# Kernel optimization log

Hardware: AMD Instinct MI355X
Metric: run time of the kernel (lower is better)

The kernel has to match this reference:

```python
import jax, jax.numpy as jnp
import numpy as np

N_NODES = 50000


def _gcn_conv(x, src, dst, W, b, n_nodes):
    # x: [N, Fin] -> h: [N, Fout]; GCN: D^-1/2 (A+I) D^-1/2 (x W) + b
    h = x @ W
    deg = jax.ops.segment_sum(jnp.ones_like(dst, dtype=h.dtype), dst,
                              num_segments=n_nodes)
    dinv = jax.lax.rsqrt(jnp.maximum(deg, 1.0))
    norm = dinv[src] * dinv[dst]                      # [E]
    msg = h[src] * norm[:, None]                      # [E, Fout] gather
    agg = jax.ops.segment_sum(msg, dst, num_segments=n_nodes)  # scatter-add
    return agg + b


def setup_inputs() -> dict:
    key = jax.random.key(0)
    k0, k1, k2, k3 = jax.random.split(key, 4)
    N, E, F_IN, H, C = N_NODES, 800000, 128, 128, 16
    x = jax.random.normal(k0, (N, F_IN), dtype=jnp.float32)
    edge_index = jax.random.randint(k1, (2, E), 0, N, dtype=jnp.int64)
    W1 = jax.random.normal(k2, (F_IN, H), dtype=jnp.float32) / np.sqrt(F_IN)
    b1 = jnp.zeros((H,), dtype=jnp.float32)
    W2 = jax.random.normal(k3, (H, C), dtype=jnp.float32) / np.sqrt(H)
    b2 = jnp.zeros((C,), dtype=jnp.float32)
    return {"x": x, "edge_index": edge_index, "W1": W1, "b1": b1,
            "W2": W2, "b2": b2}


def reference(x, edge_index, W1, b1, W2, b2):
    n = x.shape[0]
    # add self-loops (shared by both conv layers)
    loops = jnp.arange(n, dtype=edge_index.dtype)
    src = jnp.concatenate([edge_index[0], loops])
    dst = jnp.concatenate([edge_index[1], loops])
    h = _gcn_conv(x, src, dst, W1, b1, n)
    h = jax.nn.relu(h)
    # dropout p=0.5 is identity in eval mode
    h = _gcn_conv(h, src, dst, W2, b2, n)
    return jax.nn.log_softmax(h, axis=1)
```

## Files before the change

### kernel.cpp

```cpp
#include <hip/hip_runtime.h>
#include <math.h>


#define NBUCKET_SHIFT 8
#define BIN_CHUNK 4096

typedef __bf16 bf16x8 __attribute__((ext_vector_type(8)));
typedef float  f32x4  __attribute__((ext_vector_type(4)));
typedef float  f32x2  __attribute__((ext_vector_type(2)));

__device__ __forceinline__ unsigned short pack_bf16(float f) {
    unsigned u = __float_as_uint(f);
    return (unsigned short)((u + 0x7fffu + ((u >> 16) & 1u)) >> 16);
}

__device__ __forceinline__ void acc_fp8x16(f32x2* a, uint4 v) {
    a[0] += __builtin_amdgcn_cvt_pk_f32_fp8(v.x, false);
    a[1] += __builtin_amdgcn_cvt_pk_f32_fp8(v.x, true);
    a[2] += __builtin_amdgcn_cvt_pk_f32_fp8(v.y, false);
    a[3] += __builtin_amdgcn_cvt_pk_f32_fp8(v.y, true);
    a[4] += __builtin_amdgcn_cvt_pk_f32_fp8(v.z, false);
    a[5] += __builtin_amdgcn_cvt_pk_f32_fp8(v.z, true);
    a[6] += __builtin_amdgcn_cvt_pk_f32_fp8(v.w, false);
    a[7] += __builtin_amdgcn_cvt_pk_f32_fp8(v.w, true);
}

__global__ __launch_bounds__(256)
void count_wt_kernel(const int* __restrict__ dst, int* __restrict__ bktcnt,
                     int E, int nbuckets, int nbins,
                     const float* __restrict__ W, unsigned short* __restrict__ wtp) {
    const int blk = blockIdx.x;
    const int tid = threadIdx.x;
    if (blk >= nbins) {
        int idx = (blk - nbins) * 256 + tid;
        int j    = idx & 7;
        int lane = (idx >> 3) & 63;
        int ks   = (idx >> 9) & 3;
        int t    = idx >> 11;
        int n = t * 16 + (lane & 15);
        int k = ks * 32 + ((lane >> 4) << 3) + j;
        wtp[idx] = pack_bf16(W[k * 128 + n]);
        return;
    }
    __shared__ int cnt[256];
    cnt[tid] = 0;
    __syncthreads();
    const int e0 = blk * BIN_CHUNK;
    const int n = min(BIN_CHUNK, E - e0);
    for (int i = tid; i < n; i += 256)
        atomicAdd(&cnt[dst[e0 + i] >> NBUCKET_SHIFT], 1);
    __syncthreads();
    if (tid < nbuckets && cnt[tid] > 0) atomicAdd(&bktcnt[tid], cnt[tid]);
}

__global__ __launch_bounds__(256)
void bin_kernel(const int* __restrict__ src, const int* __restrict__ dst,
                const int* __restrict__ bktcnt, int* __restrict__ bcur,
                unsigned* __restrict__ pairs, int E, int nbuckets) {
    __shared__ unsigned spair[BIN_CHUNK];
    __shared__ int lcnt[256];
    __shared__ int lbase[256];
    __shared__ int sbase[256];
    const int tid = threadIdx.x;
    const int e0 = blockIdx.x * BIN_CHUNK;
    const int cnt = min(BIN_CHUNK, E - e0);

    int v = (tid < nbuckets) ? bktcnt[tid] : 0;
    sbase[tid] = v;
    lcnt[tid] = 0;
    __syncthreads();
#pragma unroll
    for (int off = 1; off < 256; off <<= 1) {
        int u = (tid >= off) ? sbase[tid - off] : 0;
        __syncthreads();
        sbase[tid] += u;
        __syncthreads();
    }
    int excl = sbase[tid] - v;
    __syncthreads();
    sbase[tid] = excl;
    __syncthreads();

    for (int i = tid; i < cnt; i += 256) {
        unsigned s = (unsigned)src[e0 + i], d = (unsigned)dst[e0 + i];
        spair[i] = (d >> NBUCKET_SHIFT) << 24 | (d & 255u) << 16 | s;
        atomicAdd(&lcnt[d >> NBUCKET_SHIFT], 1);
    }
    __syncthreads();

    if (tid < nbuckets) {
        int c = lcnt[tid];
        lbase[tid] = (c > 0) ? atomicAdd(&bcur[tid], c) : 0;
        lcnt[tid] = 0;
    }
    __syncthreads();

    for (int i = tid; i < cnt; i += 256) {
        unsigned p = spair[i];
        int b = (int)(p >> 24);
        int off = atomicAdd(&lcnt[b], 1);
        pairs[sbase[b] + lbase[b] + off] = p;
    }
}

__global__ __launch_bounds__(256)
void bucket_build_kernel(const int* __restrict__ bktcnt, const unsigned* __restrict__ pairs,
                         int* __restrict__ rowptr, float* __restrict__ dinv,
                         int* __restrict__ colsrc, int N, int E, int nbuckets) {
    __shared__ int cnt[256];
    __shared__ int sm[256];
    const int tid = threadIdx.x;
    const int blk = blockIdx.x;
    const int nb0 = blk << NBUCKET_SHIFT;

    int bv = (tid < nbuckets) ? bktcnt[tid] : 0;
    sm[tid] = bv;
    cnt[tid] = 0;
    __syncthreads();
#pragma unroll
    for (int off = 1; off < 256; off <<= 1) {
        int u = (tid >= off) ? sm[tid - off] : 0;
        __syncthreads();
        sm[tid] += u;
        __syncthreads();
    }
    __syncthreads();
    const int hi0 = sm[blk];
    const int lo = hi0 - bktcnt[blk];
    const int hi = hi0;
    __syncthreads();

    for (int i = lo + tid; i < hi; i += 256)
        atomicAdd(&cnt[(int)(pairs[i] >> 16) & 255], 1);
    __syncthreads();

    int v = cnt[tid];
    sm[tid] = v;
    __syncthreads();
#pragma unroll
    for (int off = 1; off < 256; off <<= 1) {
        int u = (tid >= off) ? sm[tid - off] : 0;
        __syncthreads();
        sm[tid] += u;
        __syncthreads();
    }
    int excl = sm[tid] - v;
    int node = nb0 + tid;
    if (node < N) {
        rowptr[node] = lo + excl;
        dinv[node] = rsqrtf((float)v + 1.0f);
    }
    __syncthreads();
    cnt[tid] = lo + excl;
    __syncthreads();
    for (int i = lo + tid; i < hi; i += 256) {
        unsigned p = pairs[i];
        int pos = atomicAdd(&cnt[(int)(p >> 16) & 255], 1);
        colsrc[pos] = (int)(p & 0xffffu);
    }
    if (blk == 0 && tid == 0) rowptr[N] = E;
}

__global__ __launch_bounds__(256)
void gemm1_mfma_kernel(const float* __restrict__ x, const unsigned short* __restrict__ wtp,
                       const float* __restrict__ dinv, unsigned* __restrict__ h1b, int N) {
    __shared__ float lds[4][16 * 132];
    const int tid = threadIdx.x, wave = tid >> 6, lane = tid & 63;
    const int q = lane >> 4, m = lane & 15;
    const int row0 = blockIdx.x * 64 + wave * 16;
    const int row = row0 + m;
    const int rowc = (row < N) ? row : (N - 1);

    f32x4 acc[8];
#pragma unroll
    for (int t = 0; t < 8; t++) acc[t] = (f32x4)0.0f;

#pragma unroll
    for (int ks = 0; ks < 4; ks++) {
        const float4* xp = (const float4*)(x + (size_t)rowc * 128 + ks * 32 + q * 8);
        float4 f0 = xp[0], f1 = xp[1];
        float fv[8] = {f0.x, f0.y, f0.z, f0.w, f1.x, f1.y, f1.z, f1.w};
        bf16x8 ah, al;
#pragma unroll
        for (int j = 0; j < 8; j++) {
            __bf16 h = (__bf16)fv[j];
            ah[j] = h;
            al[j] = (__bf16)(fv[j] - (float)h);
        }
#pragma unroll
        for (int t = 0; t < 8; t++) {
            bf16x8 b = *(const bf16x8*)(wtp + (size_t)(t * 4 + ks) * 512 + lane * 8);
            acc[t] = __builtin_amdgcn_mfma_f32_16x16x32_bf16(ah, b, acc[t], 0, 0, 0);
            acc[t] = __builtin_amdgcn_mfma_f32_16x16x32_bf16(al, b, acc[t], 0, 0, 0);
        }
    }

#pragma unroll
    for (int t = 0; t < 8; t++)
#pragma unroll
        for (int r = 0; r < 4; r++)
            lds[wave][(q * 4 + r) * 132 + t * 16 + m] = acc[t][r];
    __syncthreads();

    const int r2 = lane >> 2, j = lane & 3;
    const int orow = row0 + r2;
    if (orow < N) {
        float dv = dinv[orow];
        const float* lrow = &lds[wave][r2 * 132];
#pragma unroll
        for (int s = 0; s < 4; s++) {
            float4 a = *(const float4*)(lrow + s * 32 + j * 8);
            float4 b = *(const float4*)(lrow + s * 32 + j * 8 + 4);
            unsigned lo = __builtin_amdgcn_cvt_pk_fp8_f32(a.x * dv, a.y * dv, 0, false);
            lo = __builtin_amdgcn_cvt_pk_fp8_f32(a.z * dv, a.w * dv, lo, true);
            unsigned hi = __builtin_amdgcn_cvt_pk_fp8_f32(b.x * dv, b.y * dv, 0, false);
            hi = __builtin_amdgcn_cvt_pk_fp8_f32(b.z * dv, b.w * dv, hi, true);
            ((uint2*)h1b)[(size_t)orow * 16 + s * 4 + j] = make_uint2(lo, hi);
        }
    }
}

__global__ __launch_bounds__(256)
void l1_fused_kernel(const int* __restrict__ rowptr, const int* __restrict__ colsrc,
                     const float* __restrict__ dinv, const unsigned* __restrict__ h1b,
                     const float* __restrict__ b1, const float* __restrict__ W2,
                     float* __restrict__ h2s, int N) {
    __shared__ float rows[4][2][132];
    __shared__ float w2s[128 * 16];
    const int tid = threadIdx.x;
    const int wave = tid >> 6, lane = tid & 63;
    const int c = lane & 7;
    const int g = (lane >> 3) & 3;
    const int n = lane >> 5;
    const int d = blockIdx.x * 8 + wave * 2 + n;

    for (int i = tid; i < 512; i += 256)
        ((float4*)w2s)[i] = ((const float4*)W2)[i];

    const uint4* hq = (const uint4*)h1b;

    if (d < N) {
        f32x2 a[8];
#pragma unroll
        for (int j = 0; j < 8; j++) a[j] = (f32x2)0.0f;

        if (g == 0)
            acc_fp8x16(a, hq[(size_t)d * 8 + c]);

        int i = rowptr[d], end = rowptr[d + 1];
        for (; i + 16 <= end; i += 16) {
            int s0 = colsrc[i + g],     s1 = colsrc[i + 4 + g];
            int s2 = colsrc[i + 8 + g], s3 = colsrc[i + 12 + g];
            uint4 v0 = hq[(size_t)s0 * 8 + c];
            uint4 v1 = hq[(size_t)s1 * 8 + c];
            uint4 v2 = hq[(size_t)s2 * 8 + c];
            uint4 v3 = hq[(size_t)s3 * 8 + c];
            acc_fp8x16(a, v0); acc_fp8x16(a, v1);
            acc_fp8x16(a, v2); acc_fp8x16(a, v3);
        }
        for (; i + 4 <= end; i += 4) {
            int sx = colsrc[i + g];
            acc_fp8x16(a, hq[(size_t)sx * 8 + c]);
        }
        if (i < end && g < end - i)
            acc_fp8x16(a, hq[(size_t)colsrc[i + g] * 8 + c]);

#pragma unroll
        for (int j = 0; j < 8; j++) {
            a[j].x += __shfl_xor(a[j].x, 8, 64);
            a[j].y += __shfl_xor(a[j].y, 8, 64);
            a[j].x += __shfl_xor(a[j].x, 16, 64);
            a[j].y += __shfl_xor(a[j].y, 16, 64);
        }

        if (g == 0) {
            float dv = dinv[d];
            float* rbase = &rows[wave][n][c * 16];
#pragma unroll
            for (int t = 0; t < 4; t++) {
                float4 bb = ((const float4*)b1)[c * 4 + t];
                float4 o;
                o.x = fmaxf(a[2 * t].x * dv + bb.x, 0.0f);
                o.y = fmaxf(a[2 * t].y * dv + bb.y, 0.0f);
                o.z = fmaxf(a[2 * t + 1].x * dv + bb.z, 0.0f);
                o.w = fmaxf(a[2 * t + 1].y * dv + bb.w, 0.0f);
                *(float4*)(rbase + 4 * t) = o;
            }
        }
    }
    __syncthreads();

    const int n2 = lane >> 5, kh = (lane >> 4) & 1, col = lane & 15;
    const int d2 = blockIdx.x * 8 + wave * 2 + n2;
    if (d2 < N) {
        const float* r = &rows[wave][n2][kh * 64];
        const float* w = &w2s[kh * 64 * 16];
        float p = 0.0f;
#pragma unroll
        for (int k = 0; k < 64; k++)
            p = fmaf(r[k], w[k * 16 + col], p);
        p += __shfl_xor(p, 16, 64);
        if (kh == 0) h2s[(size_t)d2 * 16 + col] = p * dinv[d2];
    }
}

__global__ __launch_bounds__(256)
void l2_kernel(const int* __restrict__ rowptr, const int* __restrict__ colsrc,
               const float* __restrict__ dinv, const float* __restrict__ h2s,
               const float* __restrict__ b2, float* __restrict__ out, int N) {
    const int tid = threadIdx.x;
    const int wave = tid >> 6, lane = tid & 63;
    const int g = lane >> 2;
    const int c = lane & 3;
    const int d = blockIdx.x * 4 + wave;
    if (d >= N) return;
    const float4* h2q = (const float4*)h2s;

    float4 acc = make_float4(0.f, 0.f, 0.f, 0.f);
    if (g == 0) acc = h2q[d * 4 + c];
    int i = rowptr[d], end = rowptr[d + 1];
    for (; i + 16 <= end; i += 16) {
        int s = colsrc[i + g];
        float4 v = h2q[s * 4 + c];
        acc.x += v.x; acc.y += v.y; acc.z += v.z; acc.w += v.w;
    }
    if (i < end && g < end - i) {
        int s = colsrc[i + g];
        float4 v = h2q[s * 4 + c];
        acc.x += v.x; acc.y += v.y; acc.z += v.z; acc.w += v.w;
    }
#pragma unroll
    for (int off = 4; off <= 32; off <<= 1) {
        acc.x += __shfl_xor(acc.x, off, 64);
        acc.y += __shfl_xor(acc.y, off, 64);
        acc.z += __shfl_xor(acc.z, off, 64);
        acc.w += __shfl_xor(acc.w, off, 64);
    }
    float dv = dinv[d];
    float4 b = ((const float4*)b2)[c];
    float4 val = make_float4(acc.x * dv + b.x, acc.y * dv + b.y,
                             acc.z * dv + b.z, acc.w * dv + b.w);
    float m = fmaxf(fmaxf(val.x, val.y), fmaxf(val.z, val.w));
    m = fmaxf(m, __shfl_xor(m, 1, 64));
    m = fmaxf(m, __shfl_xor(m, 2, 64));
    float e = expf(val.x - m) + expf(val.y - m) + expf(val.z - m) + expf(val.w - m);
    e += __shfl_xor(e, 1, 64);
    e += __shfl_xor(e, 2, 64);
    float lse = m + logf(e);
    if (g == 0)
        ((float4*)out)[d * 4 + c] =
            make_float4(val.x - lse, val.y - lse, val.z - lse, val.w - lse);
}

extern "C" void kernel_launch(void* const* d_in, const int* in_sizes, int n_in,
                              void* d_out, int out_size, void* d_ws, size_t ws_size,
                              hipStream_t stream) {
    const float* x  = (const float*)d_in[0];
    const int*  ei  = (const int*)d_in[1];
    const float* W1 = (const float*)d_in[2];
    const float* b1 = (const float*)d_in[3];
    const float* W2 = (const float*)d_in[4];
    const float* b2 = (const float*)d_in[5];
    float* out = (float*)d_out;

    const int N = in_sizes[0] / 128;
    const int E = in_sizes[1] / 2;
    const int* src = ei;
    const int* dst = ei + E;
    const int nbuckets = (N + 255) >> NBUCKET_SHIFT;
    const int nbins = (E + BIN_CHUNK - 1) / BIN_CHUNK;

    float*          wsf     = (float*)d_ws;
    float*          dinv    = wsf;
    int*            rowptr  = (int*)(wsf + N);
    int*            bktcnt  = rowptr + N + 4;
    int*            bcur    = bktcnt + 256;
    unsigned short* wtp     = (unsigned short*)(bcur + 256);
    int*            colsrc  = bcur + 256 + 8192;
    unsigned*       pairs   = (unsigned*)(colsrc + E);
    unsigned*       h1b     = pairs + E;
    float*          h2s     = (float*)(h1b + (size_t)N * 32);

    hipMemsetAsync(bktcnt, 0, 512 * sizeof(int), stream);
    count_wt_kernel<<<nbins + 64, 256, 0, stream>>>(dst, bktcnt, E, nbuckets,
                                                    nbins, W1, wtp);
    bin_kernel<<<nbins, 256, 0, stream>>>(src, dst, bktcnt, bcur, pairs, E, nbuckets);
    bucket_build_kernel<<<nbuckets, 256, 0, stream>>>(bktcnt, pairs, rowptr,
                                                      dinv, colsrc, N, E, nbuckets);

    gemm1_mfma_kernel<<<(N + 63) / 64, 256, 0, stream>>>(x, wtp, dinv, h1b, N);

    l1_fused_kernel<<<(N + 7) / 8, 256, 0, stream>>>(rowptr, colsrc, dinv, h1b,
                                                     b1, W2, h2s, N);

    l2_kernel<<<(N + 3) / 4, 256, 0, stream>>>(rowptr, colsrc, dinv, h2s, b2, out, N);
}
```

Baseline: 188.8 us.

## Pad CSR rows to multiples of 16 with dummy zero node, software-pipeline index loads

Each row's neighbour list is padded up to a multiple of 16 entries. The padding entries point at an extra zero-filled row N appended to the h1b and h2s feature buffers. This lets the layer-1 and layer-2 aggregation loops drop their remainder/tail handling, and the layer-1 loop prefetches the next 16 column indices while the current gathers are in flight. It adds padding slots in colsrc plus extra gathers of the zero row, and needs a per-node count array and more workspace.

```diff
diff --git a/kernel.cpp b/kernel.cpp
--- a/kernel.cpp
+++ b/kernel.cpp
@@ -4,6 +4,7 @@
 
 #define NBUCKET_SHIFT 8
 #define BIN_CHUNK 4096
+#define PAD_SLOP (15 << NBUCKET_SHIFT)
 
 typedef __bf16 bf16x8 __attribute__((ext_vector_type(8)));
 typedef float  f32x4  __attribute__((ext_vector_type(4)));
@@ -105,14 +106,21 @@
 
 __global__ __launch_bounds__(256)
 void bucket_build_kernel(const int* __restrict__ bktcnt, const unsigned* __restrict__ pairs,
-                         int* __restrict__ rowptr, float* __restrict__ dinv,
-                         int* __restrict__ colsrc, int N, int E, int nbuckets) {
+                         int* __restrict__ rowptr, int* __restrict__ rowcnt,
+                         float* __restrict__ dinv, int* __restrict__ colsrc,
+                         unsigned* __restrict__ h1b, float* __restrict__ h2s,
+                         int N, int E, int nbuckets) {
     __shared__ int cnt[256];
     __shared__ int sm[256];
     const int tid = threadIdx.x;
     const int blk = blockIdx.x;
     const int nb0 = blk << NBUCKET_SHIFT;
 
+    if (blk == 0) {
+        if (tid < 32) h1b[(size_t)N * 32 + tid] = 0u;
+        else if (tid < 48) h2s[(size_t)N * 16 + (tid - 32)] = 0.0f;
+    }
+
     int bv = (tid < nbuckets) ? bktcnt[tid] : 0;
     sm[tid] = bv;
     cnt[tid] = 0;
@@ -135,7 +143,8 @@
     __syncthreads();
 
     int v = cnt[tid];
-    sm[tid] = v;
+    int pdeg = (v + 15) & ~15;
+    sm[tid] = pdeg;
     __syncthreads();
 #pragma unroll
     for (int off = 1; off < 256; off <<= 1) {
@@ -144,21 +153,25 @@
         sm[tid] += u;
         __syncthreads();
     }
-    int excl = sm[tid] - v;
+    int pexcl = sm[tid] - pdeg;
+    const int pbase = lo + blk * PAD_SLOP;
+    const int start = pbase + pexcl;
     int node = nb0 + tid;
     if (node < N) {
-        rowptr[node] = lo + excl;
+        rowptr[node] = start;
+        rowcnt[node] = pdeg;
         dinv[node] = rsqrtf((float)v + 1.0f);
     }
     __syncthreads();
-    cnt[tid] = lo + excl;
+    cnt[tid] = start;
     __syncthreads();
     for (int i = lo + tid; i < hi; i += 256) {
         unsigned p = pairs[i];
         int pos = atomicAdd(&cnt[(int)(p >> 16) & 255], 1);
         colsrc[pos] = (int)(p & 0xffffu);
     }
-    if (blk == 0 && tid == 0) rowptr[N] = E;
+    for (int p = start + v; p < start + pdeg; ++p)
+        colsrc[p] = N;
 }
 
 __global__ __launch_bounds__(256)
@@ -221,7 +234,8 @@
 }
 
 __global__ __launch_bounds__(256)
-void l1_fused_kernel(const int* __restrict__ rowptr, const int* __restrict__ colsrc,
+void l1_fused_kernel(const int* __restrict__ rowptr, const int* __restrict__ rowcnt,
+                     const int* __restrict__ colsrc,
                      const float* __restrict__ dinv, const unsigned* __restrict__ h1b,
                      const float* __restrict__ b1, const float* __restrict__ W2,
                      float* __restrict__ h2s, int N) {
@@ -247,23 +261,26 @@
         if (g == 0)
             acc_fp8x16(a, hq[(size_t)d * 8 + c]);
 
-        int i = rowptr[d], end = rowptr[d + 1];
-        for (; i + 16 <= end; i += 16) {
-            int s0 = colsrc[i + g],     s1 = colsrc[i + 4 + g];
-            int s2 = colsrc[i + 8 + g], s3 = colsrc[i + 12 + g];
+        int i = rowptr[d];
+        const int end = i + rowcnt[d];
+        int s0 = 0, s1 = 0, s2 = 0, s3 = 0;
+        if (i < end) {
+            s0 = colsrc[i + g];      s1 = colsrc[i + g + 4];
+            s2 = colsrc[i + g + 8];  s3 = colsrc[i + g + 12];
+        }
+        while (i < end) {
             uint4 v0 = hq[(size_t)s0 * 8 + c];
             uint4 v1 = hq[(size_t)s1 * 8 + c];
             uint4 v2 = hq[(size_t)s2 * 8 + c];
             uint4 v3 = hq[(size_t)s3 * 8 + c];
+            i += 16;
+            if (i < end) {
+                s0 = colsrc[i + g];      s1 = colsrc[i + g + 4];
+                s2 = colsrc[i + g + 8];  s3 = colsrc[i + g + 12];
+            }
             acc_fp8x16(a, v0); acc_fp8x16(a, v1);
             acc_fp8x16(a, v2); acc_fp8x16(a, v3);
         }
-        for (; i + 4 <= end; i += 4) {
-            int sx = colsrc[i + g];
-            acc_fp8x16(a, hq[(size_t)sx * 8 + c]);
-        }
-        if (i < end && g < end - i)
-            acc_fp8x16(a, hq[(size_t)colsrc[i + g] * 8 + c]);
 
 #pragma unroll
         for (int j = 0; j < 8; j++) {
@@ -305,7 +322,8 @@
 }
 
 __global__ __launch_bounds__(256)
-void l2_kernel(const int* __restrict__ rowptr, const int* __restrict__ colsrc,
+void l2_kernel(const int* __restrict__ rowptr, const int* __restrict__ rowcnt,
+               const int* __restrict__ colsrc,
                const float* __restrict__ dinv, const float* __restrict__ h2s,
                const float* __restrict__ b2, float* __restrict__ out, int N) {
     const int tid = threadIdx.x;
@@ -318,13 +336,9 @@
 
     float4 acc = make_float4(0.f, 0.f, 0.f, 0.f);
     if (g == 0) acc = h2q[d * 4 + c];
-    int i = rowptr[d], end = rowptr[d + 1];
-    for (; i + 16 <= end; i += 16) {
-        int s = colsrc[i + g];
-        float4 v = h2q[s * 4 + c];
-        acc.x += v.x; acc.y += v.y; acc.z += v.z; acc.w += v.w;
-    }
-    if (i < end && g < end - i) {
+    int i = rowptr[d];
+    const int end = i + rowcnt[d];
+    for (; i < end; i += 16) {
         int s = colsrc[i + g];
         float4 v = h2q[s * 4 + c];
         acc.x += v.x; acc.y += v.y; acc.z += v.z; acc.w += v.w;
@@ -369,29 +383,33 @@
     const int* dst = ei + E;
     const int nbuckets = (N + 255) >> NBUCKET_SHIFT;
     const int nbins = (E + BIN_CHUNK - 1) / BIN_CHUNK;
+    const int csz = E + nbuckets * PAD_SLOP;
 
     float*          wsf     = (float*)d_ws;
     float*          dinv    = wsf;
     int*            rowptr  = (int*)(wsf + N);
-    int*            bktcnt  = rowptr + N + 4;
+    int*            rowcnt  = rowptr + N + 4;
+    int*            bktcnt  = rowcnt + N;
     int*            bcur    = bktcnt + 256;
     unsigned short* wtp     = (unsigned short*)(bcur + 256);
     int*            colsrc  = bcur + 256 + 8192;
-    unsigned*       pairs   = (unsigned*)(colsrc + E);
+    unsigned*       pairs   = (unsigned*)(colsrc + csz);
     unsigned*       h1b     = pairs + E;
-    float*          h2s     = (float*)(h1b + (size_t)N * 32);
+    float*          h2s     = (float*)(h1b + (size_t)(N + 1) * 32);
 
     hipMemsetAsync(bktcnt, 0, 512 * sizeof(int), stream);
     count_wt_kernel<<<nbins + 64, 256, 0, stream>>>(dst, bktcnt, E, nbuckets,
                                                     nbins, W1, wtp);
     bin_kernel<<<nbins, 256, 0, stream>>>(src, dst, bktcnt, bcur, pairs, E, nbuckets);
-    bucket_build_kernel<<<nbuckets, 256, 0, stream>>>(bktcnt, pairs, rowptr,
-                                                      dinv, colsrc, N, E, nbuckets);
+    bucket_build_kernel<<<nbuckets, 256, 0, stream>>>(bktcnt, pairs, rowptr, rowcnt,
+                                                      dinv, colsrc, h1b, h2s,
+                                                      N, E, nbuckets);
 
     gemm1_mfma_kernel<<<(N + 63) / 64, 256, 0, stream>>>(x, wtp, dinv, h1b, N);
 
-    l1_fused_kernel<<<(N + 7) / 8, 256, 0, stream>>>(rowptr, colsrc, dinv, h1b,
-                                                     b1, W2, h2s, N);
-
-    l2_kernel<<<(N + 3) / 4, 256, 0, stream>>>(rowptr, colsrc, dinv, h2s, b2, out, N);
-}
+    l1_fused_kernel<<<(N + 7) / 8, 256, 0, stream>>>(rowptr, rowcnt, colsrc, dinv,
+                                                     h1b, b1, W2, h2s, N);
+
+    l2_kernel<<<(N + 3) / 4, 256, 0, stream>>>(rowptr, rowcnt, colsrc, dinv, h2s,
+                                               b2, out, N);
+}
```

New measurement: 184.1 us. 2.5% less time.
